# Kernel tuning notes

Measured on AMD Instinct MI355X. Metric: run time of the kernel, lower is better.

The kernel has to match this reference:

```python
import jax, jax.numpy as jnp
import numpy as np

H = 32          # num_attention_heads
ROPE_BASE = 10000.0


def _rotary_freqs_cis(seq_len: int, head_dim: int) -> jnp.ndarray:
    # complex e^{i * pos * theta_j}, shape [seq_len, head_dim//2]
    inv_freq = 1.0 / (ROPE_BASE ** (jnp.arange(0, head_dim, 2, dtype=jnp.float32) / head_dim))
    angles = jnp.arange(seq_len, dtype=jnp.float32)[:, None] * inv_freq[None, :]
    return jax.lax.complex(jnp.cos(angles), jnp.sin(angles))


def _apply_rotary(u: jnp.ndarray, freqs_cis: jnp.ndarray) -> jnp.ndarray:
    # u: [B, S, H, hd]; faithful to apply_rotary_emb (interleaved pairs -> complex mul)
    ur = u.astype(jnp.float32).reshape(*u.shape[:-1], -1, 2)
    uc = jax.lax.complex(ur[..., 0], ur[..., 1])
    # freqs_cis broadcast: [1, S, 1, hd//2]
    uc = uc * freqs_cis[None, :, None, :]
    return jnp.stack((jnp.real(uc), jnp.imag(uc)), axis=-1).reshape(u.shape)


def setup_inputs() -> dict:
    key = jax.random.key(0)
    ks = jax.random.split(key, 5)
    B, S, D = 1, 2048, 4096
    init_std = 0.02
    x = jax.random.normal(ks[0], (B, S, D), dtype=jnp.float32)
    wq = jax.random.normal(ks[1], (D, D), dtype=jnp.float32) * init_std
    wk = jax.random.normal(ks[2], (D, D), dtype=jnp.float32) * init_std
    wv = jax.random.normal(ks[3], (D, D), dtype=jnp.float32) * init_std
    wo = jax.random.normal(ks[4], (D, D), dtype=jnp.float32) * init_std
    return {"x": x, "wq": wq, "wk": wk, "wv": wv, "wo": wo}


def reference(x, wq, wk, wv, wo):
    B, S, D = x.shape
    hd = D // H  # head_dim = 128
    q = (x @ wq).reshape(B, S, H, hd)
    k = (x @ wk).reshape(B, S, H, hd)
    v = (x @ wv).reshape(B, S, H, hd)

    freqs_cis = _rotary_freqs_cis(S, hd)
    q = _apply_rotary(q, freqs_cis)
    k = _apply_rotary(k, freqs_cis)
    # n_rep == 1 (num_key_value_heads == num_attention_heads) -> repeat_kv is identity

    scale = 1.0 / jnp.sqrt(jnp.float32(hd))
    scores = jnp.einsum('bqhd,bkhd->bhqk', q, k) * scale  # [B, H, S, S]
    causal = jnp.tril(jnp.ones((S, S), dtype=bool))
    neg = jnp.finfo(scores.dtype).min
    scores = jnp.where(causal[None, None, :, :], scores, neg)
    probs = jax.nn.softmax(scores, axis=-1)
    attn = jnp.einsum('bhqk,bkhd->bqhd', probs, v).reshape(B, S, D)
    return attn @ wo
```

## Files before the change

kernel.cpp:

```cpp
#include <hip/hip_runtime.h>
#include <stdint.h>

#define S_LEN 2048
#define DMODEL 4096
#define NHEAD 32
#define HDIM 128

typedef __attribute__((ext_vector_type(8))) short bf16x8;
typedef __attribute__((ext_vector_type(4))) float f32x4;

__device__ __forceinline__ unsigned short f2bf(float f) {
    union { float f; unsigned u; } v; v.f = f;
    unsigned u = v.u;
    unsigned r = (u + 0x7FFFu + ((u >> 16) & 1u)) >> 16;
    return (unsigned short)r;
}
__device__ __forceinline__ float bf2f(unsigned short h) {
    union { unsigned u; float f; } v; v.u = ((unsigned)h) << 16;
    return v.f;
}

__global__ void convert_x_kernel(const float* __restrict__ x,
                                 unsigned short* __restrict__ xb, int n4) {
    int t = blockIdx.x * blockDim.x + threadIdx.x;
    if (t >= n4) return;
    float4 v = ((const float4*)x)[t];
    ushort4 o;
    o.x = f2bf(v.x); o.y = f2bf(v.y); o.z = f2bf(v.z); o.w = f2bf(v.w);
    ((ushort4*)xb)[t] = o;
}

__global__ void convert_wt_kernel(const float* __restrict__ w,
                                  unsigned short* __restrict__ wt) {
    __shared__ unsigned short t[64][65];
    int n0 = blockIdx.x * 64, k0 = blockIdx.y * 64;
    for (int i = 0; i < 16; ++i) {
        int o = threadIdx.x + i * 256;
        int r = o >> 6, c = o & 63;
        t[r][c] = f2bf(w[(size_t)(k0 + r) * DMODEL + n0 + c]);
    }
    __syncthreads();
    for (int i = 0; i < 16; ++i) {
        int o = threadIdx.x + i * 256;
        int rr = o >> 6, kk = o & 63;
        wt[(size_t)(n0 + rr) * DMODEL + k0 + kk] = t[kk][rr];
    }
}

template<int STORE_MODE>
__global__ __launch_bounds__(256, 2)
void gemm_bt_kernel(const unsigned short* __restrict__ A,
                    const unsigned short* __restrict__ BT,
                    void* __restrict__ C, int M, int N, int K) {
    __shared__ __align__(16) unsigned short As[128 * 32];
    __shared__ __align__(16) unsigned short Bs[128 * 32];
    const int lane = threadIdx.x & 63;
    const int w = threadIdx.x >> 6;
    const int wm = w & 1, wn = w >> 1;
    const int m0 = blockIdx.y * 128, n0 = blockIdx.x * 128;

    f32x4 zero = {0.f, 0.f, 0.f, 0.f};
    f32x4 acc[4][4];
    for (int i = 0; i < 4; ++i)
        for (int j = 0; j < 4; ++j) acc[i][j] = zero;

    const int lr = lane >> 2;
    const int lc = lane & 3;
    const int q = lane >> 4, lm = lane & 15;

    for (int k0 = 0; k0 < K; k0 += 32) {
        __syncthreads();
        for (int i = 0; i < 2; ++i) {
            int rb = w * 32 + i * 16;
            int r = rb + lr;
            int gc = lc ^ ((r >> 1) & 3);
            const unsigned short* ga = A + (size_t)(m0 + r) * K + k0 + gc * 8;
            __builtin_amdgcn_global_load_lds(
                (__attribute__((address_space(1))) unsigned int*)ga,
                (__attribute__((address_space(3))) unsigned int*)(&As[rb * 32]), 16, 0, 0);
            const unsigned short* gb = BT + (size_t)(n0 + r) * K + k0 + gc * 8;
            __builtin_amdgcn_global_load_lds(
                (__attribute__((address_space(1))) unsigned int*)gb,
                (__attribute__((address_space(3))) unsigned int*)(&Bs[rb * 32]), 16, 0, 0);
        }
        __syncthreads();
        bf16x8 af[4], bf[4];
        for (int t = 0; t < 4; ++t) {
            int ra = wm * 64 + t * 16 + lm;
            af[t] = *(const bf16x8*)&As[ra * 32 + ((q ^ ((ra >> 1) & 3)) * 8)];
            int rb2 = wn * 64 + t * 16 + lm;
            bf[t] = *(const bf16x8*)&Bs[rb2 * 32 + ((q ^ ((rb2 >> 1) & 3)) * 8)];
        }
        for (int mi = 0; mi < 4; ++mi)
            for (int ni = 0; ni < 4; ++ni)
                acc[mi][ni] = __builtin_amdgcn_mfma_f32_16x16x32_bf16(
                    af[mi], bf[ni], acc[mi][ni], 0, 0, 0);
    }

    for (int mi = 0; mi < 4; ++mi) {
        int mbase = m0 + wm * 64 + mi * 16 + q * 4;
        for (int ni = 0; ni < 4; ++ni) {
            int n = n0 + wn * 64 + ni * 16 + lm;
            if (STORE_MODE == 0) {
                unsigned short* Cb = (unsigned short*)C;
                for (int r = 0; r < 4; ++r)
                    Cb[(size_t)(mbase + r) * N + n] = f2bf(acc[mi][ni][r]);
            } else if (STORE_MODE == 1) {
                unsigned short* Cb = (unsigned short*)C;
                ushort4 v;
                v.x = f2bf(acc[mi][ni][0]); v.y = f2bf(acc[mi][ni][1]);
                v.z = f2bf(acc[mi][ni][2]); v.w = f2bf(acc[mi][ni][3]);
                *(ushort4*)&Cb[(size_t)n * M + mbase] = v;
            } else {
                float* Cf = (float*)C;
                for (int r = 0; r < 4; ++r)
                    Cf[(size_t)(mbase + r) * N + n] = acc[mi][ni][r];
            }
        }
    }
}

__global__ void rope_kernel(unsigned short* __restrict__ qb,
                            unsigned short* __restrict__ kb) {
    int t = blockIdx.x * blockDim.x + threadIdx.x;
    if (t >= S_LEN * DMODEL / 2) return;
    int s = t >> 11;
    int p = t & 2047;
    int j = p & 63;
    float ang = (float)s * exp2f((float)j * -0.2076205059304602f);
    float sn, cs;
    sincosf(ang, &sn, &cs);
    size_t idx = (size_t)s * DMODEL + 2 * p;
    const float SC = 0.08838834764831845f;
    float a0 = bf2f(qb[idx]), a1 = bf2f(qb[idx + 1]);
    qb[idx]     = f2bf((a0 * cs - a1 * sn) * SC);
    qb[idx + 1] = f2bf((a0 * sn + a1 * cs) * SC);
    float b0 = bf2f(kb[idx]), b1 = bf2f(kb[idx + 1]);
    kb[idx]     = f2bf(b0 * cs - b1 * sn);
    kb[idx + 1] = f2bf(b0 * sn + b1 * cs);
}

__global__ __launch_bounds__(256, 2)
void attn_kernel(const unsigned short* __restrict__ qb,
                 const unsigned short* __restrict__ kb,
                 const unsigned short* __restrict__ vt,
                 unsigned short* __restrict__ ab) {
    __shared__ __align__(16) unsigned short Ks[64 * 128];
    __shared__ __align__(16) unsigned short VTs[128 * 64];
    __shared__ __align__(16) unsigned short Pb[4][16 * 72];
    const int t = threadIdx.x;
    const int lane = t & 63;
    const int w = t >> 6;
    const int h = blockIdx.y;
    const int q0 = ((int)gridDim.x - 1 - (int)blockIdx.x) * 64;
    const int qw = q0 + w * 16;
    const int q = lane >> 4, lm = lane & 15;

    const int krow = t >> 2;
    const int kcol = t & 3;
    const int vrow = t >> 1;
    const int vcol = t & 1;

    const unsigned short* gK = kb + (size_t)krow * DMODEL + h * HDIM;
    const unsigned short* gV = vt + (size_t)(h * HDIM + vrow) * S_LEN;

    bf16x8 qf[4];
    for (int kc = 0; kc < 4; ++kc)
        qf[kc] = *(const bf16x8*)&qb[(size_t)(qw + lm) * DMODEL + h * HDIM + kc * 32 + q * 8];

    f32x4 zero = {0.f, 0.f, 0.f, 0.f};
    f32x4 o[8];
    for (int i = 0; i < 8; ++i) o[i] = zero;
    float mrow[4] = {-1e30f, -1e30f, -1e30f, -1e30f};
    float lrow[4] = {0.f, 0.f, 0.f, 0.f};

    const int nch = q0 / 64 + 1;

    bf16x8 kreg[4], vreg[4];
    for (int i = 0; i < 4; ++i) {
        kreg[i] = *(const bf16x8*)&gK[(size_t)0 * DMODEL + (kcol + i * 4) * 8];
        vreg[i] = *(const bf16x8*)&gV[0 + (vcol + i * 2) * 8];
    }
    for (int i = 0; i < 4; ++i) {
        *(bf16x8*)&Ks[krow * 128 + (((kcol + i * 4) ^ (krow & 15)) * 8)] = kreg[i];
        *(bf16x8*)&VTs[vrow * 64 + (((vcol + i * 2) ^ (vrow & 7)) * 8)] = vreg[i];
    }
    __syncthreads();

    for (int c = 0; c < nch; ++c) {
        const int j0 = c * 64;
        if (c + 1 < nch) {
            const size_t jn = (size_t)(j0 + 64);
            for (int i = 0; i < 4; ++i) {
                kreg[i] = *(const bf16x8*)&gK[jn * DMODEL + (kcol + i * 4) * 8];
                vreg[i] = *(const bf16x8*)&gV[jn + (vcol + i * 2) * 8];
            }
        }

        f32x4 s[4];
        for (int ks = 0; ks < 4; ++ks) s[ks] = zero;
        for (int kc = 0; kc < 4; ++kc)
            for (int ks = 0; ks < 4; ++ks) {
                bf16x8 kf = *(const bf16x8*)&Ks[(ks * 16 + lm) * 128 + (((kc * 4 + q) ^ lm) * 8)];
                s[ks] = __builtin_amdgcn_mfma_f32_16x16x32_bf16(qf[kc], kf, s[ks], 0, 0, 0);
            }
        if (c == nch - 1) {
            for (int ks = 0; ks < 4; ++ks)
                for (int r = 0; r < 4; ++r)
                    if (j0 + ks * 16 + lm > qw + q * 4 + r) s[ks][r] = -1e30f;
        }
        float al[4];
        for (int r = 0; r < 4; ++r) {
            float mx = fmaxf(fmaxf(s[0][r], s[1][r]), fmaxf(s[2][r], s[3][r]));
            mx = fmaxf(mx, __shfl_xor(mx, 1));
            mx = fmaxf(mx, __shfl_xor(mx, 2));
            mx = fmaxf(mx, __shfl_xor(mx, 4));
            mx = fmaxf(mx, __shfl_xor(mx, 8));
            float mn = fmaxf(mrow[r], mx);
            al[r] = __expf(mrow[r] - mn);
            mrow[r] = mn;
            float rs = 0.f;
            float pv[4];
            for (int ks = 0; ks < 4; ++ks) {
                pv[ks] = __expf(s[ks][r] - mn);
                rs += pv[ks];
            }
            rs += __shfl_xor(rs, 1);
            rs += __shfl_xor(rs, 2);
            rs += __shfl_xor(rs, 4);
            rs += __shfl_xor(rs, 8);
            lrow[r] = lrow[r] * al[r] + rs;
            for (int ks = 0; ks < 4; ++ks)
                Pb[w][(q * 4 + r) * 72 + ks * 16 + lm] = f2bf(pv[ks]);
        }
        bf16x8 pA0 = *(const bf16x8*)&Pb[w][lm * 72 + q * 8];
        bf16x8 pA1 = *(const bf16x8*)&Pb[w][lm * 72 + 32 + q * 8];
        for (int nt = 0; nt < 8; ++nt) {
            int d = nt * 16 + lm;
            bf16x8 vf0 = *(const bf16x8*)&VTs[d * 64 + ((q ^ (d & 7)) * 8)];
            bf16x8 vf1 = *(const bf16x8*)&VTs[d * 64 + (((4 + q) ^ (d & 7)) * 8)];
            f32x4 oo = o[nt];
            for (int r = 0; r < 4; ++r) oo[r] *= al[r];
            oo = __builtin_amdgcn_mfma_f32_16x16x32_bf16(pA0, vf0, oo, 0, 0, 0);
            o[nt] = __builtin_amdgcn_mfma_f32_16x16x32_bf16(pA1, vf1, oo, 0, 0, 0);
        }

        __syncthreads();
        if (c + 1 < nch) {
            for (int i = 0; i < 4; ++i) {
                *(bf16x8*)&Ks[krow * 128 + (((kcol + i * 4) ^ (krow & 15)) * 8)] = kreg[i];
                *(bf16x8*)&VTs[vrow * 64 + (((vcol + i * 2) ^ (vrow & 7)) * 8)] = vreg[i];
            }
        }
        __syncthreads();
    }

    float inv[4];
    for (int r = 0; r < 4; ++r) inv[r] = 1.0f / lrow[r];
    for (int nt = 0; nt < 8; ++nt) {
        int d = h * HDIM + lm + nt * 16;
        for (int r = 0; r < 4; ++r)
            ab[(size_t)(qw + q * 4 + r) * DMODEL + d] = f2bf(o[nt][r] * inv[r]);
    }
}

extern "C" void kernel_launch(void* const* d_in, const int* in_sizes, int n_in,
                              void* d_out, int out_size, void* d_ws, size_t ws_size,
                              hipStream_t stream) {
    const float* x  = (const float*)d_in[0];
    const float* wq = (const float*)d_in[1];
    const float* wk = (const float*)d_in[2];
    const float* wv = (const float*)d_in[3];
    const float* wo = (const float*)d_in[4];
    char* ws = (char*)d_ws;
    const size_t MB = 1024 * 1024;
    unsigned short* xb  = (unsigned short*)(ws + 0 * MB);
    unsigned short* qb  = (unsigned short*)(ws + 16 * MB);
    unsigned short* kb  = (unsigned short*)(ws + 32 * MB);
    unsigned short* vtb = (unsigned short*)(ws + 48 * MB);
    unsigned short* ab  = (unsigned short*)(ws + 64 * MB);
    unsigned short* wtb = (unsigned short*)(ws + 80 * MB);

    dim3 cg(64, 64);
    dim3 gg(32, 16);

    convert_x_kernel<<<(S_LEN * DMODEL / 4) / 256, 256, 0, stream>>>(x, xb, S_LEN * DMODEL / 4);

    convert_wt_kernel<<<cg, 256, 0, stream>>>(wq, wtb);
    gemm_bt_kernel<0><<<gg, 256, 0, stream>>>(xb, wtb, qb, S_LEN, DMODEL, DMODEL);
    convert_wt_kernel<<<cg, 256, 0, stream>>>(wk, wtb);
    gemm_bt_kernel<0><<<gg, 256, 0, stream>>>(xb, wtb, kb, S_LEN, DMODEL, DMODEL);
    convert_wt_kernel<<<cg, 256, 0, stream>>>(wv, wtb);
    gemm_bt_kernel<1><<<gg, 256, 0, stream>>>(xb, wtb, vtb, S_LEN, DMODEL, DMODEL);

    rope_kernel<<<(S_LEN * DMODEL / 2) / 256, 256, 0, stream>>>(qb, kb);

    attn_kernel<<<dim3(S_LEN / 64, NHEAD), 256, 0, stream>>>(qb, kb, vtb, ab);

    convert_wt_kernel<<<cg, 256, 0, stream>>>(wo, wtb);
    gemm_bt_kernel<2><<<gg, 256, 0, stream>>>(ab, wtb, d_out, S_LEN, DMODEL, DMODEL);
}
```

Before: 801.9 us.

## Load K/V fragments directly from global into registers, fuse Q RoPE into attention

The attention kernel drops its shared-memory K and V tiles and block-wide barriers. Each wave now loads its MFMA K and V fragments straight from global memory (L2) into registers, prefetching the next K chunk. The row-sum of P is computed with an MFMA against a ones vector instead of shuffle reductions, and the Q rotary embedding and scaling move into the attention prologue, so the separate RoPE pass only touches K. The cost is redundant global and L2 traffic: all four waves in a block load the same K/V. Register pressure also rises (32 extra bf16x8 fragments), which may reduce occupancy.

```diff
diff --git a/kernel.cpp b/kernel.cpp
--- a/kernel.cpp
+++ b/kernel.cpp
@@ -120,8 +120,7 @@
     }
 }
 
-__global__ void rope_kernel(unsigned short* __restrict__ qb,
-                            unsigned short* __restrict__ kb) {
+__global__ void rope_k_kernel(unsigned short* __restrict__ kb) {
     int t = blockIdx.x * blockDim.x + threadIdx.x;
     if (t >= S_LEN * DMODEL / 2) return;
     int s = t >> 11;
@@ -131,10 +130,6 @@
     float sn, cs;
     sincosf(ang, &sn, &cs);
     size_t idx = (size_t)s * DMODEL + 2 * p;
-    const float SC = 0.08838834764831845f;
-    float a0 = bf2f(qb[idx]), a1 = bf2f(qb[idx + 1]);
-    qb[idx]     = f2bf((a0 * cs - a1 * sn) * SC);
-    qb[idx + 1] = f2bf((a0 * sn + a1 * cs) * SC);
     float b0 = bf2f(kb[idx]), b1 = bf2f(kb[idx + 1]);
     kb[idx]     = f2bf(b0 * cs - b1 * sn);
     kb[idx + 1] = f2bf(b0 * sn + b1 * cs);
@@ -145,8 +140,6 @@
                  const unsigned short* __restrict__ kb,
                  const unsigned short* __restrict__ vt,
                  unsigned short* __restrict__ ab) {
-    __shared__ __align__(16) unsigned short Ks[64 * 128];
-    __shared__ __align__(16) unsigned short VTs[128 * 64];
     __shared__ __align__(16) unsigned short Pb[4][16 * 72];
     const int t = threadIdx.x;
     const int lane = t & 63;
@@ -156,60 +149,89 @@
     const int qw = q0 + w * 16;
     const int q = lane >> 4, lm = lane & 15;
 
-    const int krow = t >> 2;
-    const int kcol = t & 3;
-    const int vrow = t >> 1;
-    const int vcol = t & 1;
-
-    const unsigned short* gK = kb + (size_t)krow * DMODEL + h * HDIM;
-    const unsigned short* gV = vt + (size_t)(h * HDIM + vrow) * S_LEN;
-
     bf16x8 qf[4];
-    for (int kc = 0; kc < 4; ++kc)
-        qf[kc] = *(const bf16x8*)&qb[(size_t)(qw + lm) * DMODEL + h * HDIM + kc * 32 + q * 8];
+    {
+        const int s = qw + lm;
+        const unsigned short* gq = qb + (size_t)s * DMODEL + h * HDIM + q * 8;
+        const float SC = 0.08838834764831845f;
+#pragma unroll
+        for (int kc = 0; kc < 4; ++kc) {
+            bf16x8 raw = *(const bf16x8*)&gq[kc * 32];
+            bf16x8 ov;
+#pragma unroll
+            for (int tt = 0; tt < 4; ++tt) {
+                int p = kc * 16 + q * 4 + tt;
+                float ang = (float)s * exp2f((float)p * -0.2076205059304602f);
+                float sn, cs;
+                sincosf(ang, &sn, &cs);
+                float a0 = bf2f((unsigned short)raw[2 * tt]);
+                float a1 = bf2f((unsigned short)raw[2 * tt + 1]);
+                ov[2 * tt]     = (short)f2bf((a0 * cs - a1 * sn) * SC);
+                ov[2 * tt + 1] = (short)f2bf((a0 * sn + a1 * cs) * SC);
+            }
+            qf[kc] = ov;
+        }
+    }
+
+    const unsigned short* gK = kb + (size_t)lm * DMODEL + h * HDIM + q * 8;
+    const unsigned short* gV = vt + (size_t)(h * HDIM + lm) * S_LEN + q * 8;
 
     f32x4 zero = {0.f, 0.f, 0.f, 0.f};
     f32x4 o[8];
+#pragma unroll
     for (int i = 0; i < 8; ++i) o[i] = zero;
+    f32x4 ls = zero;
     float mrow[4] = {-1e30f, -1e30f, -1e30f, -1e30f};
-    float lrow[4] = {0.f, 0.f, 0.f, 0.f};
+
+    bf16x8 ones;
+#pragma unroll
+    for (int i = 0; i < 8; ++i) ones[i] = (short)0x3F80;
 
     const int nch = q0 / 64 + 1;
 
-    bf16x8 kreg[4], vreg[4];
-    for (int i = 0; i < 4; ++i) {
-        kreg[i] = *(const bf16x8*)&gK[(size_t)0 * DMODEL + (kcol + i * 4) * 8];
-        vreg[i] = *(const bf16x8*)&gV[0 + (vcol + i * 2) * 8];
-    }
-    for (int i = 0; i < 4; ++i) {
-        *(bf16x8*)&Ks[krow * 128 + (((kcol + i * 4) ^ (krow & 15)) * 8)] = kreg[i];
-        *(bf16x8*)&VTs[vrow * 64 + (((vcol + i * 2) ^ (vrow & 7)) * 8)] = vreg[i];
-    }
-    __syncthreads();
+    bf16x8 kf[16], vf[16];
+#pragma unroll
+    for (int ks = 0; ks < 4; ++ks)
+#pragma unroll
+        for (int kc = 0; kc < 4; ++kc)
+            kf[ks * 4 + kc] = *(const bf16x8*)&gK[(size_t)(ks * 16) * DMODEL + kc * 32];
 
     for (int c = 0; c < nch; ++c) {
         const int j0 = c * 64;
+#pragma unroll
+        for (int nt = 0; nt < 8; ++nt)
+#pragma unroll
+            for (int hf = 0; hf < 2; ++hf)
+                vf[nt * 2 + hf] = *(const bf16x8*)&gV[(size_t)(nt * 16) * S_LEN + j0 + hf * 32];
+
+        f32x4 s[4];
+#pragma unroll
+        for (int ks = 0; ks < 4; ++ks) s[ks] = zero;
+#pragma unroll
+        for (int kc = 0; kc < 4; ++kc)
+#pragma unroll
+            for (int ks = 0; ks < 4; ++ks)
+                s[ks] = __builtin_amdgcn_mfma_f32_16x16x32_bf16(qf[kc], kf[ks * 4 + kc], s[ks], 0, 0, 0);
+
         if (c + 1 < nch) {
             const size_t jn = (size_t)(j0 + 64);
-            for (int i = 0; i < 4; ++i) {
-                kreg[i] = *(const bf16x8*)&gK[jn * DMODEL + (kcol + i * 4) * 8];
-                vreg[i] = *(const bf16x8*)&gV[jn + (vcol + i * 2) * 8];
-            }
-        }
-
-        f32x4 s[4];
-        for (int ks = 0; ks < 4; ++ks) s[ks] = zero;
-        for (int kc = 0; kc < 4; ++kc)
-            for (int ks = 0; ks < 4; ++ks) {
-                bf16x8 kf = *(const bf16x8*)&Ks[(ks * 16 + lm) * 128 + (((kc * 4 + q) ^ lm) * 8)];
-                s[ks] = __builtin_amdgcn_mfma_f32_16x16x32_bf16(qf[kc], kf, s[ks], 0, 0, 0);
-            }
+#pragma unroll
+            for (int ks = 0; ks < 4; ++ks)
+#pragma unroll
+                for (int kc = 0; kc < 4; ++kc)
+                    kf[ks * 4 + kc] = *(const bf16x8*)&gK[(jn + ks * 16) * DMODEL + kc * 32];
+        }
+
         if (c == nch - 1) {
+#pragma unroll
             for (int ks = 0; ks < 4; ++ks)
+#pragma unroll
                 for (int r = 0; r < 4; ++r)
                     if (j0 + ks * 16 + lm > qw + q * 4 + r) s[ks][r] = -1e30f;
         }
+
         float al[4];
+#pragma unroll
         for (int r = 0; r < 4; ++r) {
             float mx = fmaxf(fmaxf(s[0][r], s[1][r]), fmaxf(s[2][r], s[3][r]));
             mx = fmaxf(mx, __shfl_xor(mx, 1));
@@ -219,46 +241,35 @@
             float mn = fmaxf(mrow[r], mx);
             al[r] = __expf(mrow[r] - mn);
             mrow[r] = mn;
-            float rs = 0.f;
-            float pv[4];
-            for (int ks = 0; ks < 4; ++ks) {
-                pv[ks] = __expf(s[ks][r] - mn);
-                rs += pv[ks];
-            }
-            rs += __shfl_xor(rs, 1);
-            rs += __shfl_xor(rs, 2);
-            rs += __shfl_xor(rs, 4);
-            rs += __shfl_xor(rs, 8);
-            lrow[r] = lrow[r] * al[r] + rs;
+#pragma unroll
             for (int ks = 0; ks < 4; ++ks)
-                Pb[w][(q * 4 + r) * 72 + ks * 16 + lm] = f2bf(pv[ks]);
+                Pb[w][(q * 4 + r) * 72 + ks * 16 + lm] = f2bf(__expf(s[ks][r] - mn));
         }
         bf16x8 pA0 = *(const bf16x8*)&Pb[w][lm * 72 + q * 8];
         bf16x8 pA1 = *(const bf16x8*)&Pb[w][lm * 72 + 32 + q * 8];
+
+        f32x4 lss = ls;
+#pragma unroll
+        for (int r = 0; r < 4; ++r) lss[r] *= al[r];
+        lss = __builtin_amdgcn_mfma_f32_16x16x32_bf16(pA0, ones, lss, 0, 0, 0);
+        ls = __builtin_amdgcn_mfma_f32_16x16x32_bf16(pA1, ones, lss, 0, 0, 0);
+#pragma unroll
         for (int nt = 0; nt < 8; ++nt) {
-            int d = nt * 16 + lm;
-            bf16x8 vf0 = *(const bf16x8*)&VTs[d * 64 + ((q ^ (d & 7)) * 8)];
-            bf16x8 vf1 = *(const bf16x8*)&VTs[d * 64 + (((4 + q) ^ (d & 7)) * 8)];
             f32x4 oo = o[nt];
+#pragma unroll
             for (int r = 0; r < 4; ++r) oo[r] *= al[r];
-            oo = __builtin_amdgcn_mfma_f32_16x16x32_bf16(pA0, vf0, oo, 0, 0, 0);
-            o[nt] = __builtin_amdgcn_mfma_f32_16x16x32_bf16(pA1, vf1, oo, 0, 0, 0);
-        }
-
-        __syncthreads();
-        if (c + 1 < nch) {
-            for (int i = 0; i < 4; ++i) {
-                *(bf16x8*)&Ks[krow * 128 + (((kcol + i * 4) ^ (krow & 15)) * 8)] = kreg[i];
-                *(bf16x8*)&VTs[vrow * 64 + (((vcol + i * 2) ^ (vrow & 7)) * 8)] = vreg[i];
-            }
-        }
-        __syncthreads();
+            oo = __builtin_amdgcn_mfma_f32_16x16x32_bf16(pA0, vf[nt * 2 + 0], oo, 0, 0, 0);
+            o[nt] = __builtin_amdgcn_mfma_f32_16x16x32_bf16(pA1, vf[nt * 2 + 1], oo, 0, 0, 0);
+        }
     }
 
     float inv[4];
-    for (int r = 0; r < 4; ++r) inv[r] = 1.0f / lrow[r];
+#pragma unroll
+    for (int r = 0; r < 4; ++r) inv[r] = 1.0f / ls[r];
+#pragma unroll
     for (int nt = 0; nt < 8; ++nt) {
         int d = h * HDIM + lm + nt * 16;
+#pragma unroll
         for (int r = 0; r < 4; ++r)
             ab[(size_t)(qw + q * 4 + r) * DMODEL + d] = f2bf(o[nt][r] * inv[r]);
     }
@@ -293,7 +304,7 @@
     convert_wt_kernel<<<cg, 256, 0, stream>>>(wv, wtb);
     gemm_bt_kernel<1><<<gg, 256, 0, stream>>>(xb, wtb, vtb, S_LEN, DMODEL, DMODEL);
 
-    rope_kernel<<<(S_LEN * DMODEL / 2) / 256, 256, 0, stream>>>(qb, kb);
+    rope_k_kernel<<<(S_LEN * DMODEL / 2) / 256, 256, 0, stream>>>(kb);
 
     attn_kernel<<<dim3(S_LEN / 64, NHEAD), 256, 0, stream>>>(qb, kb, vtb, ab);
 
```

New measurement: 1.075 ms. +34.0%, slower.
